# Optimization experiments

Hardware: AMD Instinct MI355X
Metric: run time of the kernel (lower is better)

The kernel has to match this reference:

```python
import jax, jax.numpy as jnp
import numpy as np

H = 64   # hid_dim (hard-coded in Attn_LSTM)
C = 8    # enc_in / out_dim
L = 96   # enc_seq_len = interval*lag = max_length
T = 24   # pre_len = window*horizon
B = 4096


def _p(key, shape, scale=0.1):
    return (jax.random.normal(key, shape, dtype=jnp.float32) * scale)


def setup_inputs() -> dict:
    key = jax.random.key(0)
    ks = jax.random.split(key, 20)
    inp = {
        'x_enc': jax.random.normal(ks[0], (B, L, C), dtype=jnp.float32),
        'x_mark_enc': jax.random.normal(ks[1], (B, L, 4), dtype=jnp.float32),
        'x_dec': jax.random.normal(ks[2], (B, T, C), dtype=jnp.float32),
        'x_mark_dec': jax.random.normal(ks[3], (B, T, 4), dtype=jnp.float32),
        # encoder LSTM (1 layer, input C -> hid H), pytorch gate order i,f,g,o
        'enc_Wih': _p(ks[4], (4 * H, C)), 'enc_Whh': _p(ks[5], (4 * H, H)),
        'enc_bih': _p(ks[6], (4 * H,)), 'enc_bhh': _p(ks[7], (4 * H,)),
        # decoder
        'emb_W': _p(ks[8], (H, C)), 'emb_b': _p(ks[9], (H,)),
        'attn_W': _p(ks[10], (L, 2 * H)), 'attn_b': _p(ks[11], (L,)),
        'comb_W': _p(ks[12], (H, 2 * H)), 'comb_b': _p(ks[13], (H,)),
        'dec_Wih': _p(ks[14], (4 * H, H)), 'dec_Whh': _p(ks[15], (4 * H, H)),
        'dec_bih': _p(ks[16], (4 * H,)), 'dec_bhh': _p(ks[17], (4 * H,)),
        'out_W': _p(ks[18], (C, H)), 'out_b': _p(ks[19], (C,)),
    }
    return inp


def _lstm_cell(x, h, c, Wih, Whh, bih, bhh):
    g = x @ Wih.T + h @ Whh.T + (bih + bhh)
    i, f, gg, o = jnp.split(g, 4, axis=-1)
    i, f, o = jax.nn.sigmoid(i), jax.nn.sigmoid(f), jax.nn.sigmoid(o)
    c_new = f * c + i * jnp.tanh(gg)
    h_new = o * jnp.tanh(c_new)
    return h_new, c_new


def _forward(x_enc, enc_Wih, enc_Whh, enc_bih, enc_bhh,
             emb_W, emb_b, attn_W, attn_b, comb_W, comb_b,
             dec_Wih, dec_Whh, dec_bih, dec_bhh, out_W, out_b):
    seq_last = x_enc[:, -1:, :]               # [B,1,C]
    x = x_enc - seq_last                      # normalized

    # ---- encoder: 1-layer LSTM over L steps ----
    h0 = jnp.zeros((x.shape[0], H), dtype=x.dtype)
    c0 = jnp.zeros_like(h0)

    def enc_step(carry, xt):
        h, c = carry
        h, c = _lstm_cell(xt, h, c, enc_Wih, enc_Whh, enc_bih, enc_bhh)
        return (h, c), h

    (h_enc, c_enc), enc_out = jax.lax.scan(enc_step, (h0, c0),
                                           jnp.swapaxes(x, 0, 1))
    enc_out = jnp.swapaxes(enc_out, 0, 1)     # [B,L,H]

    # ---- attention decoder: T sequential steps ----
    dec_in0 = x[:, -1, :]                     # last (normalized) input, [B,C]

    def dec_step(carry, _):
        inp, h, c = carry
        emb = jax.nn.relu(inp @ emb_W.T + emb_b)                       # [B,H]
        aw = jax.nn.softmax(jnp.concatenate([emb, h], -1) @ attn_W.T + attn_b)  # [B,L]
        ctx = jnp.einsum('bl,blh->bh', aw, enc_out)                    # [B,H]
        comb = jnp.concatenate([emb, ctx], -1) @ comb_W.T + comb_b     # [B,H]
        h, c = _lstm_cell(comb, h, c, dec_Wih, dec_Whh, dec_bih, dec_bhh)
        pred = h @ out_W.T + out_b                                     # [B,C]
        # original code feeds prediction.detach() back in
        return (jax.lax.stop_gradient(pred), h, c), (pred, aw)

    _, (preds, aws) = jax.lax.scan(dec_step, (dec_in0, h_enc, c_enc),
                                   None, length=T)
    pre_y = jnp.swapaxes(preds, 0, 1) + seq_last   # [B,T,C]
    return pre_y


def reference(x_enc, x_mark_enc, x_dec, x_mark_dec,
              enc_Wih, enc_Whh, enc_bih, enc_bhh,
              emb_W, emb_b, attn_W, attn_b, comb_W, comb_b,
              dec_Wih, dec_Whh, dec_bih, dec_bhh, out_W, out_b):
    # x_mark_enc, x_dec, x_mark_dec are accepted but unused (as in original)
    return _forward(x_enc, enc_Wih, enc_Whh, enc_bih, enc_bhh,
                    emb_W, emb_b, attn_W, attn_b, comb_W, comb_b,
                    dec_Wih, dec_Whh, dec_bih, dec_bhh, out_W, out_b)
```

## Files before the change

### kernel.cpp

```cpp
#include <hip/hip_runtime.h>

#define LL 96
#define TT 24
#define HH 64
#define CC 8
#define GG 256
#define BT 8
#define NB 512

typedef unsigned short u16t;
typedef unsigned int   u32t;
typedef __attribute__((ext_vector_type(8))) short bf16x8;
typedef __attribute__((ext_vector_type(4))) float f32x4;

__device__ __forceinline__ float b2f(u16t u){ union{u32t i; float f;} v; v.i=((u32t)u)<<16; return v.f; }
__device__ __forceinline__ float lo2f(u32t p){ union{u32t i; float f;} v; v.i=p<<16; return v.f; }
__device__ __forceinline__ float hi2f(u32t p){ union{u32t i; float f;} v; v.i=p&0xffff0000u; return v.f; }
__device__ __forceinline__ u16t f2b(float f){ union{float f; u32t i;} v; v.f=f; u32t l=(v.i>>16)&1u; v.i+=0x7fffu+l; return (u16t)(v.i>>16); }
__device__ __forceinline__ float rcpf(float x){ return __builtin_amdgcn_rcpf(x); }
__device__ __forceinline__ float sigm(float x){ return rcpf(1.f + __expf(-x)); }
__device__ __forceinline__ float tanh2(float x){ return 1.f - 2.f*rcpf(__expf(2.f*x) + 1.f); }
__device__ __forceinline__ u32t pk2(float a, float b){ return (u32t)f2b(a) | ((u32t)f2b(b)<<16); }
__device__ __forceinline__ bf16x8 u2b8(uint4 u){ union{uint4 a; bf16x8 b;} v; v.a=u; return v.b; }
__device__ __forceinline__ int aaddr(int k, int m){ return (((k>>5)*4 + ((k>>3)&3))*16 + m)*8 + (k&7); }

template<bool F32> __device__ __forceinline__ float ldf(const void* p, size_t i){
    if constexpr (F32) return ((const float*)p)[i];
    else               return b2f(((const u16t*)p)[i]);
}
template<bool F32> __device__ __forceinline__ uint4 ld8p(const void* p, size_t i){
    if constexpr (F32){
        const float* f = (const float*)p + i;
        uint4 r; r.x = pk2(f[0],f[1]); r.y = pk2(f[2],f[3]);
                 r.z = pk2(f[4],f[5]); r.w = pk2(f[6],f[7]);
        return r;
    } else return *(const uint4*)((const u16t*)p + i);
}
template<bool F32> __device__ __forceinline__ void stf(void* p, size_t i, float v){
    if constexpr (F32) ((float*)p)[i] = v;
    else               ((u16t*)p)[i] = f2b(v);
}
template<bool F32> __device__ __forceinline__ float ldW_enc(const void* wih, const void* whh, int r, int k){
    if (k < CC)      return ldf<F32>(wih, (size_t)r*CC + k);
    else if (k < 72) return ldf<F32>(whh, (size_t)r*HH + (k-CC));
    else             return 0.f;
}

__device__ __forceinline__ bool inputs_are_f32(const void* bih){
    const u16t* p = (const u16t*)bih;
    int cnt = 0;
    #pragma unroll
    for (int i = 0; i < 64; ++i){
        u32t e = ((u32t)p[i] >> 7) & 0xFFu;
        cnt += (e >= 128u) ? 1 : 0;
    }
    return cnt > 0;
}

template<bool F32>
__global__ __launch_bounds__(256,2) void fused_g(
    const void* __restrict__ x_enc,
    const void* __restrict__ eWih, const void* __restrict__ eWhh,
    const void* __restrict__ ebih, const void* __restrict__ ebhh,
    const void* __restrict__ embW, const void* __restrict__ embb,
    const void* __restrict__ attnW, const void* __restrict__ attnb,
    const void* __restrict__ combW, const void* __restrict__ combb,
    const void* __restrict__ dWih, const void* __restrict__ dWhh,
    const void* __restrict__ dbih, const void* __restrict__ dbhh,
    const void* __restrict__ outW, const void* __restrict__ outb,
    void* __restrict__ outp, u16t* __restrict__ eoG)
{
    if (inputs_are_f32(ebih) != F32) return;

    __shared__ __align__(16) float slp[CC*10];
    __shared__ __align__(16) short Abuf2[2][1536];
    __shared__ __align__(16) char  uni[18880];

    const int tid = threadIdx.x;
    const int b0  = blockIdx.x * BT;
    const int col = tid & 15, quad = (tid >> 4) & 3, wv = tid >> 6;
    const int r0  = (quad >> 1) * 2;

    bf16x8 Bf[4][3];
    float  biasg[4];
    #pragma unroll
    for (int g = 0; g < 4; ++g){
        int r = g*64 + wv*16 + col;
        biasg[g] = ldf<F32>(ebih, r) + ldf<F32>(ebhh, r);
        #pragma unroll
        for (int kb = 0; kb < 3; ++kb){
            bf16x8 v;
            #pragma unroll
            for (int x = 0; x < 8; ++x){
                int k = kb*32 + quad*8 + x;
                v[x] = (short)f2b(ldW_enc<F32>(eWih, eWhh, r, k));
            }
            Bf[g][kb] = v;
        }
    }
    for (int n = tid; n < 2*1536; n += 256) ((short*)Abuf2)[n] = 0;
    float sl = 0.f; size_t xbase = 0;
    if (tid < BT*CC){ int b = tid >> 3, i = tid & 7;
        xbase = (size_t)(b0+b)*(LL*CC) + i;
        sl = ldf<F32>(x_enc, xbase + (size_t)(LL-1)*CC);
        slp[i*10 + b] = sl; }
    __syncthreads();
    if (tid < BT*CC){ short v = (short)f2b(ldf<F32>(x_enc, xbase) - sl);
        Abuf2[0][tid] = v; Abuf2[0][tid + 64] = v; }
    float xr = (tid < BT*CC) ? ldf<F32>(x_enc, xbase + CC) : 0.f;

    const int jmy = wv*16 + col;
    const int kh  = 8 + jmy;
    const int hwbase = aaddr(kh, 0);

    u32t ebase[2];
    #pragma unroll
    for (int rr = 0; rr < 2; ++rr){
        u32t bg = (u32t)(b0 + ((quad*4 + r0 + rr) & 7));
        ebase[rr] = (bg*4u + (u32t)(jmy>>4))*1536u + (u32t)((jmy&15)*8);
    }

    float creg[2] = {0.f,0.f};
    u16t  hb16[2] = {0,0};

    for (int t = 0; t < LL; ++t){
        __syncthreads();
        const bf16x8* AbR = (const bf16x8*)Abuf2[t & 1];
        short*        AbW = Abuf2[(t + 1) & 1];
        bf16x8 a0 = AbR[(0*4 + quad)*16 + col];
        bf16x8 a1 = AbR[(1*4 + quad)*16 + col];
        bf16x8 a2 = AbR[(2*4 + quad)*16 + col];
        f32x4 acc[4];
        #pragma unroll
        for (int g = 0; g < 4; ++g){
            f32x4 a; a[0]=biasg[g]; a[1]=biasg[g]; a[2]=biasg[g]; a[3]=biasg[g];
            a = __builtin_amdgcn_mfma_f32_16x16x32_bf16(a0, Bf[g][0], a, 0,0,0);
            a = __builtin_amdgcn_mfma_f32_16x16x32_bf16(a1, Bf[g][1], a, 0,0,0);
            a = __builtin_amdgcn_mfma_f32_16x16x32_bf16(a2, Bf[g][2], a, 0,0,0);
            acc[g] = a;
        }
        int off = (t>>5)*512 + ((t>>3)&3)*128 + (t&7);
        #pragma unroll
        for (int rr = 0; rr < 2; ++rr){
            int r = r0 + rr;
            int b = (quad*4 + r) & 7;
            float c = sigm(acc[1][r])*creg[rr] + sigm(acc[0][r])*tanh2(acc[2][r]);
            float h = sigm(acc[3][r])*tanh2(c);
            creg[rr] = c; hb16[rr] = f2b(h);
            eoG[ebase[rr] + off] = hb16[rr];
            AbW[hwbase + b*8]     = (short)hb16[rr];
            AbW[hwbase + (b+8)*8] = (short)hb16[rr];
        }
        if (tid < BT*CC && t < LL-1){
            short v = (short)f2b(xr - sl);
            AbW[tid] = v; AbW[tid + 64] = v;
            int tn = (t+2 < LL) ? t+2 : LL-1;
            xr = ldf<F32>(x_enc, xbase + (size_t)tn*CC);
        }
    }

    bf16x8 Bd[4][4];
    #pragma unroll
    for (int g = 0; g < 4; ++g){
        int r = g*64 + wv*16 + col;
        Bd[g][0] = u2b8(ld8p<F32>(dWih, (size_t)r*HH + quad*8));
        Bd[g][1] = u2b8(ld8p<F32>(dWih, (size_t)r*HH + 32 + quad*8));
        Bd[g][2] = u2b8(ld8p<F32>(dWhh, (size_t)r*HH + quad*8));
        Bd[g][3] = u2b8(ld8p<F32>(dWhh, (size_t)r*HH + 32 + quad*8));
    }
    bf16x8 Ba[2][4];
    #pragma unroll
    for (int kb = 0; kb < 4; ++kb)
        Ba[0][kb] = u2b8(ld8p<F32>(attnW, (size_t)(wv*16+col)*128 + kb*32 + quad*8));
    if (wv < 2){
        #pragma unroll
        for (int kb = 0; kb < 4; ++kb)
            Ba[1][kb] = u2b8(ld8p<F32>(attnW, (size_t)((4+wv)*16+col)*128 + kb*32 + quad*8));
    } else {
        #pragma unroll
        for (int kb = 0; kb < 4; ++kb) Ba[1][kb] = Ba[0][kb];
    }
    bf16x8 Bc[4];
    #pragma unroll
    for (int kb = 0; kb < 4; ++kb)
        Bc[kb] = u2b8(ld8p<F32>(combW, (size_t)(wv*16+col)*128 + kb*32 + quad*8));
    bf16x8 zz = {0,0,0,0,0,0,0,0};
    bf16x8 eBf = zz;
    if (quad == 0) eBf = u2b8(ld8p<F32>(embW, (size_t)(wv*16+col)*CC));
    bf16x8 oBf0 = zz, oBf1 = zz;
    if (col < CC){
        oBf0 = u2b8(ld8p<F32>(outW, (size_t)col*HH + quad*8));
        oBf1 = u2b8(ld8p<F32>(outW, (size_t)col*HH + 32 + quad*8));
    }

    float* decB  = (float*)(uni + 0);
    float* attnB = (float*)(uni + 1024);
    float* embB  = (float*)(uni + 1408);
    float* combB = (float*)(uni + 1664);
    float* outB  = (float*)(uni + 1920);
    float* Lg    = (float*)(uni + 1952);
    u16t*  awB   = (u16t*)(uni + 5024);
    u16t*  Ae    = (u16t*)(uni + 6560);
    u16t*  Ah0   = (u16t*)(uni + 8608);
    u16t*  Ah1   = (u16t*)(uni + 10656);
    u16t*  Actx  = (u16t*)(uni + 12704);
    u16t*  Acmb  = (u16t*)(uni + 14752);
    u16t*  Apred = (u16t*)(uni + 16800);

    #pragma unroll
    for (int rr = 0; rr < 2; ++rr){
        int b = (quad*4 + r0 + rr) & 7;
        Ah0[aaddr(jmy, b)]     = hb16[rr];
        Ah0[aaddr(jmy, b+8)]   = hb16[rr];
    }
    decB[tid] = ldf<F32>(dbih, tid) + ldf<F32>(dbhh, tid);
    if (tid < LL) attnB[tid] = ldf<F32>(attnb, tid);
    if (tid < HH) embB[tid]  = ldf<F32>(embb, tid);
    if (tid < HH) combB[tid] = ldf<F32>(combb, tid);
    if (tid < CC) outB[tid]  = ldf<F32>(outb, tid);
    for (int n = tid; n < 1024; n += 256) Apred[n] = 0;
    __syncthreads();

    const u16t* ebp = eoG + (size_t)(b0 + wv*2) * 6144;
    uint4 eF0[12], eF1[12];
    #pragma unroll
    for (int f = 0; f < 12; ++f) eF0[f] = *(const uint4*)(ebp + f*512 + quad*128 + col*8);
    #pragma unroll
    for (int f = 0; f < 12; ++f) eF1[f] = *(const uint4*)(ebp + 6144 + f*512 + quad*128 + col*8);

    const int lgS = tid & 31, bS = tid >> 5;
    const bf16x8* AeV   = (const bf16x8*)Ae;
    const bf16x8* ActxV = (const bf16x8*)Actx;
    const bf16x8* AcmbV = (const bf16x8*)Acmb;
    const bf16x8* ApV   = (const bf16x8*)Apred;

    for (int t = 0; t < TT; ++t){
        u16t* AhR = (t & 1) ? Ah1 : Ah0;
        u16t* AhW = (t & 1) ? Ah0 : Ah1;
        const bf16x8* AhV = (const bf16x8*)AhR;

        {
            bf16x8 ap = ApV[quad*16 + col];
            float eb = embB[wv*16 + col];
            f32x4 a; a[0]=eb; a[1]=eb; a[2]=eb; a[3]=eb;
            a = __builtin_amdgcn_mfma_f32_16x16x32_bf16(ap, eBf, a, 0,0,0);
            #pragma unroll
            for (int r = 0; r < 4; ++r)
                Ae[aaddr(wv*16+col, quad*4 + r)] = f2b(fmaxf(a[r], 0.f));
        }
        __syncthreads();

        {
            bf16x8 ae0 = AeV[(0*4+quad)*16 + col], ae1 = AeV[(1*4+quad)*16 + col];
            bf16x8 ah0 = AhV[(0*4+quad)*16 + col], ah1 = AhV[(1*4+quad)*16 + col];
            const int ns = (wv < 2) ? 2 : 1;
            for (int s = 0; s < ns; ++s){
                int lt = (s == 0) ? wv : 4+wv;
                float bz = attnB[lt*16 + col];
                f32x4 a; a[0]=bz; a[1]=bz; a[2]=bz; a[3]=bz;
                a = __builtin_amdgcn_mfma_f32_16x16x32_bf16(ae0, Ba[s][0], a, 0,0,0);
                a = __builtin_amdgcn_mfma_f32_16x16x32_bf16(ae1, Ba[s][1], a, 0,0,0);
                a = __builtin_amdgcn_mfma_f32_16x16x32_bf16(ah0, Ba[s][2], a, 0,0,0);
                a = __builtin_amdgcn_mfma_f32_16x16x32_bf16(ah1, Ba[s][3], a, 0,0,0);
                if (quad < 2)
                    *(float4*)&Lg[(lt*16+col)*8 + quad*4] = make_float4(a[0],a[1],a[2],a[3]);
            }
        }
        __syncthreads();

        {
            int l = lgS*3;
            float ev0 = Lg[l*8 + bS], ev1 = Lg[(l+1)*8 + bS], ev2 = Lg[(l+2)*8 + bS];
            float mx = fmaxf(ev0, fmaxf(ev1, ev2));
            #pragma unroll
            for (int m = 16; m >= 1; m >>= 1) mx = fmaxf(mx, __shfl_xor(mx, m, 32));
            float e0 = __expf(ev0 - mx), e1 = __expf(ev1 - mx), e2 = __expf(ev2 - mx);
            float sm = e0 + e1 + e2;
            #pragma unroll
            for (int m = 16; m >= 1; m >>= 1) sm += __shfl_xor(sm, m, 32);
            float inv = rcpf(sm);
            awB[bS*96 + l]     = f2b(e0*inv);
            awB[bS*96 + l + 1] = f2b(e1*inv);
            awB[bS*96 + l + 2] = f2b(e2*inv);
        }
        {
            const u16t* ap0 = awB + (wv*2)*96;
            bf16x8 f0 = *(const bf16x8*)(ap0 + quad*8);
            bf16x8 f1 = *(const bf16x8*)(ap0 + 32 + quad*8);
            bf16x8 f2 = *(const bf16x8*)(ap0 + 64 + quad*8);
            #pragma unroll
            for (int nt = 0; nt < 4; ++nt){
                f32x4 a; a[0]=0.f; a[1]=0.f; a[2]=0.f; a[3]=0.f;
                a = __builtin_amdgcn_mfma_f32_16x16x32_bf16(f0, u2b8(eF0[nt*3+0]), a, 0,0,0);
                a = __builtin_amdgcn_mfma_f32_16x16x32_bf16(f1, u2b8(eF0[nt*3+1]), a, 0,0,0);
                a = __builtin_amdgcn_mfma_f32_16x16x32_bf16(f2, u2b8(eF0[nt*3+2]), a, 0,0,0);
                if (quad == 0){
                    u16t v = f2b(a[0]);
                    Actx[aaddr(nt*16+col, wv*2)]   = v;
                    Actx[aaddr(nt*16+col, wv*2+8)] = v;
                }
            }
            const u16t* ap1 = awB + (wv*2+1)*96;
            bf16x8 g0 = *(const bf16x8*)(ap1 + quad*8);
            bf16x8 g1 = *(const bf16x8*)(ap1 + 32 + quad*8);
            bf16x8 g2 = *(const bf16x8*)(ap1 + 64 + quad*8);
            #pragma unroll
            for (int nt = 0; nt < 4; ++nt){
                f32x4 a; a[0]=0.f; a[1]=0.f; a[2]=0.f; a[3]=0.f;
                a = __builtin_amdgcn_mfma_f32_16x16x32_bf16(g0, u2b8(eF1[nt*3+0]), a, 0,0,0);
                a = __builtin_amdgcn_mfma_f32_16x16x32_bf16(g1, u2b8(eF1[nt*3+1]), a, 0,0,0);
                a = __builtin_amdgcn_mfma_f32_16x16x32_bf16(g2, u2b8(eF1[nt*3+2]), a, 0,0,0);
                if (quad == 0){
                    u16t v = f2b(a[0]);
                    Actx[aaddr(nt*16+col, wv*2+1)] = v;
                    Actx[aaddr(nt*16+col, wv*2+9)] = v;
                }
            }
        }
        __syncthreads();

        {
            bf16x8 ae0 = AeV[(0*4+quad)*16 + col],   ae1 = AeV[(1*4+quad)*16 + col];
            bf16x8 ax0 = ActxV[(0*4+quad)*16 + col], ax1 = ActxV[(1*4+quad)*16 + col];
            float bz = combB[wv*16 + col];
            f32x4 a; a[0]=bz; a[1]=bz; a[2]=bz; a[3]=bz;
            a = __builtin_amdgcn_mfma_f32_16x16x32_bf16(ae0, Bc[0], a, 0,0,0);
            a = __builtin_amdgcn_mfma_f32_16x16x32_bf16(ae1, Bc[1], a, 0,0,0);
            a = __builtin_amdgcn_mfma_f32_16x16x32_bf16(ax0, Bc[2], a, 0,0,0);
            a = __builtin_amdgcn_mfma_f32_16x16x32_bf16(ax1, Bc[3], a, 0,0,0);
            #pragma unroll
            for (int r = 0; r < 4; ++r)
                Acmb[aaddr(wv*16+col, quad*4 + r)] = f2b(a[r]);
        }
        __syncthreads();

        {
            bf16x8 ac0 = AcmbV[(0*4+quad)*16 + col], ac1 = AcmbV[(1*4+quad)*16 + col];
            bf16x8 ah0 = AhV[(0*4+quad)*16 + col],   ah1 = AhV[(1*4+quad)*16 + col];
            f32x4 g4[4];
            #pragma unroll
            for (int g = 0; g < 4; ++g){
                float bz = decB[g*64 + wv*16 + col];
                f32x4 a; a[0]=bz; a[1]=bz; a[2]=bz; a[3]=bz;
                a = __builtin_amdgcn_mfma_f32_16x16x32_bf16(ac0, Bd[g][0], a, 0,0,0);
                a = __builtin_amdgcn_mfma_f32_16x16x32_bf16(ac1, Bd[g][1], a, 0,0,0);
                a = __builtin_amdgcn_mfma_f32_16x16x32_bf16(ah0, Bd[g][2], a, 0,0,0);
                a = __builtin_amdgcn_mfma_f32_16x16x32_bf16(ah1, Bd[g][3], a, 0,0,0);
                g4[g] = a;
            }
            #pragma unroll
            for (int rr = 0; rr < 2; ++rr){
                int r = r0 + rr;
                int b = (quad*4 + r) & 7;
                float c = sigm(g4[1][r])*creg[rr] + sigm(g4[0][r])*tanh2(g4[2][r]);
                float h = sigm(g4[3][r])*tanh2(c);
                creg[rr] = c;
                u16t hv = f2b(h);
                AhW[aaddr(jmy, b)]   = hv;
                AhW[aaddr(jmy, b+8)] = hv;
            }
        }
        __syncthreads();

        if (wv == 0){
            const bf16x8* AhWV = (const bf16x8*)AhW;
            bf16x8 xh0 = AhWV[(0*4+quad)*16 + col];
            bf16x8 xh1 = AhWV[(1*4+quad)*16 + col];
            float ob = outB[col & 7];
            f32x4 a; a[0]=ob; a[1]=ob; a[2]=ob; a[3]=ob;
            a = __builtin_amdgcn_mfma_f32_16x16x32_bf16(xh0, oBf0, a, 0,0,0);
            a = __builtin_amdgcn_mfma_f32_16x16x32_bf16(xh1, oBf1, a, 0,0,0);
            if (col < CC){
                #pragma unroll
                for (int r = 0; r < 4; ++r){
                    int m = quad*4 + r, b = m & 7;
                    float p = a[r];
                    Apred[aaddr(col, m)] = f2b(p);
                    if (m < 8)
                        stf<F32>(outp, ((size_t)(b0+b)*TT + t)*CC + col, p + slp[col*10 + b]);
                }
            }
        }
        __syncthreads();
    }
}

extern "C" void kernel_launch(void* const* d_in, const int* in_sizes, int n_in,
                              void* d_out, int out_size, void* d_ws, size_t ws_size,
                              hipStream_t stream)
{
    (void)in_sizes; (void)n_in; (void)out_size; (void)ws_size;
    fused_g<false><<<NB, 256, 0, stream>>>(
        d_in[0],
        d_in[4],  d_in[5],  d_in[6],  d_in[7],
        d_in[8],  d_in[9],  d_in[10], d_in[11],
        d_in[12], d_in[13], d_in[14], d_in[15],
        d_in[16], d_in[17], d_in[18], d_in[19],
        d_out, (u16t*)d_ws);
    fused_g<true><<<NB, 256, 0, stream>>>(
        d_in[0],
        d_in[4],  d_in[5],  d_in[6],  d_in[7],
        d_in[8],  d_in[9],  d_in[10], d_in[11],
        d_in[12], d_in[13], d_in[14], d_in[15],
        d_in[16], d_in[17], d_in[18], d_in[19],
        d_out, (u16t*)d_ws);
}
```

Measured before the change: 292.6 us.

## Fold output projection into decoder embedding and prestage encoder inputs in LDS

The decoder's pred→embedding chain is algebraically folded: emb = relu(h·(embW·outW)ᵀ + embW·outb + embb), computed directly from the previous hidden state. This removes the separate output-projection stage and one barrier per decoder step, and the output store for step t-1 moves into the next step's embedding phase. The encoder input sequence is now normalised and packed into LDS up front, and each step's global store of the encoder hidden state is deferred to after the next barrier. Together these shorten the serial per-step dependency chain, at the cost of extra LDS and a composite weight built per thread at startup with an extra bf16 rounding.

```diff
diff --git a/kernel.cpp b/kernel.cpp
--- a/kernel.cpp
+++ b/kernel.cpp
@@ -74,7 +74,8 @@
 
     __shared__ __align__(16) float slp[CC*10];
     __shared__ __align__(16) short Abuf2[2][1536];
-    __shared__ __align__(16) char  uni[18880];
+    __shared__ __align__(16) u16t  xls[LL*64];
+    __shared__ __align__(16) char  uni[16576];
 
     const int tid = threadIdx.x;
     const int b0  = blockIdx.x * BT;
@@ -99,15 +100,23 @@
         }
     }
     for (int n = tid; n < 2*1536; n += 256) ((short*)Abuf2)[n] = 0;
-    float sl = 0.f; size_t xbase = 0;
     if (tid < BT*CC){ int b = tid >> 3, i = tid & 7;
-        xbase = (size_t)(b0+b)*(LL*CC) + i;
-        sl = ldf<F32>(x_enc, xbase + (size_t)(LL-1)*CC);
-        slp[i*10 + b] = sl; }
+        slp[i*10 + b] = ldf<F32>(x_enc, (size_t)(b0+b)*(LL*CC) + (LL-1)*CC + i); }
     __syncthreads();
-    if (tid < BT*CC){ short v = (short)f2b(ldf<F32>(x_enc, xbase) - sl);
+
+    for (int n = tid; n < BT*LL; n += 256){
+        int b = n / LL, t = n - b*LL;
+        uint4 p = ld8p<F32>(x_enc, ((size_t)(b0+b)*LL + t)*CC);
+        uint4 q;
+        q.x = pk2(lo2f(p.x) - slp[0*10+b], hi2f(p.x) - slp[1*10+b]);
+        q.y = pk2(lo2f(p.y) - slp[2*10+b], hi2f(p.y) - slp[3*10+b]);
+        q.z = pk2(lo2f(p.z) - slp[4*10+b], hi2f(p.z) - slp[5*10+b]);
+        q.w = pk2(lo2f(p.w) - slp[6*10+b], hi2f(p.w) - slp[7*10+b]);
+        *(uint4*)(xls + t*64 + b*8) = q;
+    }
+    __syncthreads();
+    if (tid < BT*CC){ short v = (short)xls[tid];
         Abuf2[0][tid] = v; Abuf2[0][tid + 64] = v; }
-    float xr = (tid < BT*CC) ? ldf<F32>(x_enc, xbase + CC) : 0.f;
 
     const int jmy = wv*16 + col;
     const int kh  = 8 + jmy;
@@ -121,10 +130,15 @@
     }
 
     float creg[2] = {0.f,0.f};
-    u16t  hb16[2] = {0,0};
+    u16t  hprev[2] = {0,0};
+    u32t  offprev = 0;
 
     for (int t = 0; t < LL; ++t){
         __syncthreads();
+        if (t > 0){
+            eoG[ebase[0] + offprev] = hprev[0];
+            eoG[ebase[1] + offprev] = hprev[1];
+        }
         const bf16x8* AbR = (const bf16x8*)Abuf2[t & 1];
         short*        AbW = Abuf2[(t + 1) & 1];
         bf16x8 a0 = AbR[(0*4 + quad)*16 + col];
@@ -139,25 +153,25 @@
             a = __builtin_amdgcn_mfma_f32_16x16x32_bf16(a2, Bf[g][2], a, 0,0,0);
             acc[g] = a;
         }
-        int off = (t>>5)*512 + ((t>>3)&3)*128 + (t&7);
+        u32t off = (u32t)((t>>5)*512 + ((t>>3)&3)*128 + (t&7));
         #pragma unroll
         for (int rr = 0; rr < 2; ++rr){
             int r = r0 + rr;
             int b = (quad*4 + r) & 7;
             float c = sigm(acc[1][r])*creg[rr] + sigm(acc[0][r])*tanh2(acc[2][r]);
             float h = sigm(acc[3][r])*tanh2(c);
-            creg[rr] = c; hb16[rr] = f2b(h);
-            eoG[ebase[rr] + off] = hb16[rr];
-            AbW[hwbase + b*8]     = (short)hb16[rr];
-            AbW[hwbase + (b+8)*8] = (short)hb16[rr];
-        }
+            creg[rr] = c; hprev[rr] = f2b(h);
+            AbW[hwbase + b*8]     = (short)hprev[rr];
+            AbW[hwbase + (b+8)*8] = (short)hprev[rr];
+        }
+        offprev = off;
         if (tid < BT*CC && t < LL-1){
-            short v = (short)f2b(xr - sl);
+            short v = (short)xls[(t+1)*64 + tid];
             AbW[tid] = v; AbW[tid + 64] = v;
-            int tn = (t+2 < LL) ? t+2 : LL-1;
-            xr = ldf<F32>(x_enc, xbase + (size_t)tn*CC);
-        }
-    }
+        }
+    }
+    eoG[ebase[0] + offprev] = hprev[0];
+    eoG[ebase[1] + offprev] = hprev[1];
 
     bf16x8 Bd[4][4];
     #pragma unroll
@@ -185,40 +199,60 @@
     for (int kb = 0; kb < 4; ++kb)
         Bc[kb] = u2b8(ld8p<F32>(combW, (size_t)(wv*16+col)*128 + kb*32 + quad*8));
     bf16x8 zz = {0,0,0,0,0,0,0,0};
-    bf16x8 eBf = zz;
-    if (quad == 0) eBf = u2b8(ld8p<F32>(embW, (size_t)(wv*16+col)*CC));
     bf16x8 oBf0 = zz, oBf1 = zz;
     if (col < CC){
         oBf0 = u2b8(ld8p<F32>(outW, (size_t)col*HH + quad*8));
         oBf1 = u2b8(ld8p<F32>(outW, (size_t)col*HH + 32 + quad*8));
     }
+    bf16x8 wpf[2];
+    float  bprime;
+    u16t   e0bu;
+    {
+        int n = wv*16 + col;
+        #pragma unroll
+        for (int kb = 0; kb < 2; ++kb){
+            bf16x8 v;
+            #pragma unroll
+            for (int x = 0; x < 8; ++x){
+                int j = kb*32 + quad*8 + x;
+                float s = 0.f;
+                #pragma unroll
+                for (int i = 0; i < CC; ++i)
+                    s += ldf<F32>(outW, (size_t)i*HH + j) * ldf<F32>(embW, (size_t)n*CC + i);
+                v[x] = (short)f2b(s);
+            }
+            wpf[kb] = v;
+        }
+        float bp = ldf<F32>(embb, n);
+        #pragma unroll
+        for (int i = 0; i < CC; ++i)
+            bp += ldf<F32>(outb, i) * ldf<F32>(embW, (size_t)n*CC + i);
+        bprime = bp;
+        e0bu = f2b(fmaxf(ldf<F32>(embb, n), 0.f));
+    }
 
     float* decB  = (float*)(uni + 0);
     float* attnB = (float*)(uni + 1024);
-    float* embB  = (float*)(uni + 1408);
-    float* combB = (float*)(uni + 1664);
-    float* outB  = (float*)(uni + 1920);
-    float* Lg    = (float*)(uni + 1952);
-    u16t*  awB   = (u16t*)(uni + 5024);
-    u16t*  Ae    = (u16t*)(uni + 6560);
-    u16t*  Ah0   = (u16t*)(uni + 8608);
-    u16t*  Ah1   = (u16t*)(uni + 10656);
-    u16t*  Actx  = (u16t*)(uni + 12704);
-    u16t*  Acmb  = (u16t*)(uni + 14752);
-    u16t*  Apred = (u16t*)(uni + 16800);
+    float* combB = (float*)(uni + 1408);
+    float* outB  = (float*)(uni + 1664);
+    float* Lg    = (float*)(uni + 1728);
+    u16t*  awB   = (u16t*)(uni + 4800);
+    u16t*  Ae    = (u16t*)(uni + 6336);
+    u16t*  Ah0   = (u16t*)(uni + 8384);
+    u16t*  Ah1   = (u16t*)(uni + 10432);
+    u16t*  Actx  = (u16t*)(uni + 12480);
+    u16t*  Acmb  = (u16t*)(uni + 14528);
 
     #pragma unroll
     for (int rr = 0; rr < 2; ++rr){
         int b = (quad*4 + r0 + rr) & 7;
-        Ah0[aaddr(jmy, b)]     = hb16[rr];
-        Ah0[aaddr(jmy, b+8)]   = hb16[rr];
+        Ah0[aaddr(jmy, b)]   = hprev[rr];
+        Ah0[aaddr(jmy, b+8)] = hprev[rr];
     }
     decB[tid] = ldf<F32>(dbih, tid) + ldf<F32>(dbhh, tid);
     if (tid < LL) attnB[tid] = ldf<F32>(attnb, tid);
-    if (tid < HH) embB[tid]  = ldf<F32>(embb, tid);
     if (tid < HH) combB[tid] = ldf<F32>(combb, tid);
     if (tid < CC) outB[tid]  = ldf<F32>(outb, tid);
-    for (int n = tid; n < 1024; n += 256) Apred[n] = 0;
     __syncthreads();
 
     const u16t* ebp = eoG + (size_t)(b0 + wv*2) * 6144;
@@ -232,7 +266,6 @@
     const bf16x8* AeV   = (const bf16x8*)Ae;
     const bf16x8* ActxV = (const bf16x8*)Actx;
     const bf16x8* AcmbV = (const bf16x8*)Acmb;
-    const bf16x8* ApV   = (const bf16x8*)Apred;
 
     for (int t = 0; t < TT; ++t){
         u16t* AhR = (t & 1) ? Ah1 : Ah0;
@@ -240,13 +273,35 @@
         const bf16x8* AhV = (const bf16x8*)AhR;
 
         {
-            bf16x8 ap = ApV[quad*16 + col];
-            float eb = embB[wv*16 + col];
-            f32x4 a; a[0]=eb; a[1]=eb; a[2]=eb; a[3]=eb;
-            a = __builtin_amdgcn_mfma_f32_16x16x32_bf16(ap, eBf, a, 0,0,0);
-            #pragma unroll
-            for (int r = 0; r < 4; ++r)
-                Ae[aaddr(wv*16+col, quad*4 + r)] = f2b(fmaxf(a[r], 0.f));
+            bf16x8 h0 = AhV[(0*4+quad)*16 + col];
+            bf16x8 h1 = AhV[(1*4+quad)*16 + col];
+            if (t == 0){
+                #pragma unroll
+                for (int r = 0; r < 4; ++r)
+                    Ae[aaddr(wv*16+col, quad*4 + r)] = e0bu;
+            } else {
+                f32x4 a; a[0]=bprime; a[1]=bprime; a[2]=bprime; a[3]=bprime;
+                a = __builtin_amdgcn_mfma_f32_16x16x32_bf16(h0, wpf[0], a, 0,0,0);
+                a = __builtin_amdgcn_mfma_f32_16x16x32_bf16(h1, wpf[1], a, 0,0,0);
+                #pragma unroll
+                for (int r = 0; r < 4; ++r)
+                    Ae[aaddr(wv*16+col, quad*4 + r)] = f2b(fmaxf(a[r], 0.f));
+            }
+            if (wv == 3 && t > 0){
+                float ob = outB[col & 7];
+                f32x4 a; a[0]=ob; a[1]=ob; a[2]=ob; a[3]=ob;
+                a = __builtin_amdgcn_mfma_f32_16x16x32_bf16(h0, oBf0, a, 0,0,0);
+                a = __builtin_amdgcn_mfma_f32_16x16x32_bf16(h1, oBf1, a, 0,0,0);
+                if (col < CC){
+                    #pragma unroll
+                    for (int r = 0; r < 4; ++r){
+                        int m = quad*4 + r;
+                        if (m < 8)
+                            stf<F32>(outp, ((size_t)(b0+m)*TT + (t-1))*CC + col,
+                                     a[r] + slp[col*10 + m]);
+                    }
+                }
+            }
         }
         __syncthreads();
 
@@ -361,27 +416,25 @@
             }
         }
         __syncthreads();
-
-        if (wv == 0){
-            const bf16x8* AhWV = (const bf16x8*)AhW;
-            bf16x8 xh0 = AhWV[(0*4+quad)*16 + col];
-            bf16x8 xh1 = AhWV[(1*4+quad)*16 + col];
-            float ob = outB[col & 7];
-            f32x4 a; a[0]=ob; a[1]=ob; a[2]=ob; a[3]=ob;
-            a = __builtin_amdgcn_mfma_f32_16x16x32_bf16(xh0, oBf0, a, 0,0,0);
-            a = __builtin_amdgcn_mfma_f32_16x16x32_bf16(xh1, oBf1, a, 0,0,0);
-            if (col < CC){
-                #pragma unroll
-                for (int r = 0; r < 4; ++r){
-                    int m = quad*4 + r, b = m & 7;
-                    float p = a[r];
-                    Apred[aaddr(col, m)] = f2b(p);
-                    if (m < 8)
-                        stf<F32>(outp, ((size_t)(b0+b)*TT + t)*CC + col, p + slp[col*10 + b]);
-                }
-            }
-        }
-        __syncthreads();
+    }
+
+    if (wv == 3){
+        const bf16x8* AhV = (const bf16x8*)Ah0;
+        bf16x8 h0 = AhV[(0*4+quad)*16 + col];
+        bf16x8 h1 = AhV[(1*4+quad)*16 + col];
+        float ob = outB[col & 7];
+        f32x4 a; a[0]=ob; a[1]=ob; a[2]=ob; a[3]=ob;
+        a = __builtin_amdgcn_mfma_f32_16x16x32_bf16(h0, oBf0, a, 0,0,0);
+        a = __builtin_amdgcn_mfma_f32_16x16x32_bf16(h1, oBf1, a, 0,0,0);
+        if (col < CC){
+            #pragma unroll
+            for (int r = 0; r < 4; ++r){
+                int m = quad*4 + r;
+                if (m < 8)
+                    stf<F32>(outp, ((size_t)(b0+m)*TT + (TT-1))*CC + col,
+                             a[r] + slp[col*10 + m]);
+            }
+        }
     }
 }
 
```

After: 336.1 us. +14.9%, slower.
